# Optimization experiments

Measured on AMD Instinct MI355X. Metric: run time of the kernel, lower is better.

Reference implementation:

```python
import jax, jax.numpy as jnp
import numpy as np

NODES = 14      # input_size: nodes per graph
IN_F = 24       # seq_len: node feature dim
HID1 = 32
HID2 = 64       # hid_feats
HEADS = 2
OUT = 24        # output_size
B = 2048        # number of graphs
SLOPE = 0.2


def _make_edges():
    # fully connected (no self loops) within each 14-node graph
    pairs = np.array([(i, j) for i in range(NODES) for j in range(NODES) if i != j]).T  # [2,182]
    offs = (np.arange(B) * NODES)[:, None]
    src = (pairs[0][None, :] + offs).reshape(-1)
    dst = (pairs[1][None, :] + offs).reshape(-1)
    return np.stack([src, dst]).astype(np.int32)  # [2, 372736]


def setup_inputs() -> dict:
    key = jax.random.key(0)
    ks = jax.random.split(key, 16)
    N = B * NODES
    x = jax.random.normal(ks[0], (N, IN_F), dtype=jnp.float32)
    y = jax.random.normal(ks[1], (N, OUT), dtype=jnp.float32)
    edge_index = jnp.asarray(_make_edges())
    batch = jnp.repeat(jnp.arange(B, dtype=jnp.int32), NODES)
    s = 0.1
    params = dict(
        W1=jax.random.normal(ks[2], (IN_F, HEADS * HID1), dtype=jnp.float32) * s,
        a_src1=jax.random.normal(ks[3], (HEADS, HID1), dtype=jnp.float32) * s,
        a_dst1=jax.random.normal(ks[4], (HEADS, HID1), dtype=jnp.float32) * s,
        b1=jnp.zeros((HID1,), dtype=jnp.float32),
        W2=jax.random.normal(ks[5], (HID1, HEADS * HID2), dtype=jnp.float32) * s,
        a_src2=jax.random.normal(ks[6], (HEADS, HID2), dtype=jnp.float32) * s,
        a_dst2=jax.random.normal(ks[7], (HEADS, HID2), dtype=jnp.float32) * s,
        b2=jnp.zeros((HID2,), dtype=jnp.float32),
        Wf1=jax.random.normal(ks[8], (NODES, HID2, 8), dtype=jnp.float32) * s,
        bf1=jnp.zeros((NODES, 8), dtype=jnp.float32),
        Wf2=jax.random.normal(ks[9], (NODES, 8, OUT), dtype=jnp.float32) * s,
        bf2=jnp.zeros((NODES, OUT), dtype=jnp.float32),
    )
    return {"x": x, "y": y, "edge_index": edge_index, "batch": batch, **params}


def gat_conv(x, src, dst, W, a_src, a_dst, b):
    # PyG GATConv, concat=False (mean over heads), self-loops already in src/dst
    N = x.shape[0]
    H, F = a_src.shape
    xh = (x @ W).reshape(N, H, F)                       # [N,H,F]
    al_s = (xh * a_src).sum(-1)                         # [N,H]
    al_d = (xh * a_dst).sum(-1)                         # [N,H]
    alpha = jax.nn.leaky_relu(al_s[src] + al_d[dst], SLOPE)  # [E,H]
    amax = jax.ops.segment_max(alpha, dst, num_segments=N)
    ex = jnp.exp(alpha - amax[dst])
    den = jax.ops.segment_sum(ex, dst, num_segments=N)
    w = ex / den[dst]                                   # softmax per target node
    out = jax.ops.segment_sum(w[:, :, None] * xh[src], dst, num_segments=N)  # [N,H,F]
    return out.mean(axis=1) + b


def reference(x, y, edge_index, batch, W1, a_src1, a_dst1, b1, W2, a_src2, a_dst2, b2, Wf1, bf1, Wf2, bf2):
    N = x.shape[0]
    loops = jnp.arange(N, dtype=edge_index.dtype)
    src = jnp.concatenate([edge_index[0], loops])
    dst = jnp.concatenate([edge_index[1], loops])
    h = jax.nn.elu(gat_conv(x, src, dst, W1, a_src1, a_dst1, b1))   # [N,32]
    h = gat_conv(h, src, dst, W2, a_src2, a_dst2, b2)               # [N,64]
    # batch regroup: batch ids are contiguous per graph, so the Python
    # gather-loop in the original is exactly a reshape
    nb = N // NODES
    xg = h.reshape(nb, NODES, HID2).transpose(1, 0, 2)   # [14, B, 64]
    yg = y.reshape(nb, NODES, OUT)                       # [B, 14, out]
    # per-node-index MLP ensemble, batched over the 14 indices
    hh = jax.nn.relu(jnp.einsum('kbh,kho->kbo', xg, Wf1) + bf1[:, None, :])
    pred = jax.nn.sigmoid(jnp.einsum('kbo,kop->kbp', hh, Wf2) + bf2[:, None, :])  # [14,B,out]
    return pred, yg
```

## Files before the change

### kernel.cpp

```cpp
#include <hip/hip_runtime.h>

#define NODES 14
#define IN_F 24
#define HID1 32
#define HID2 64
#define OUT_F 24
#define SLOPE 0.2f

#define XS_S 28
#define H1_S 36
#define H2_S 68

#define U_US1 0
#define U_UD1 48
#define U_US2 96
#define U_UD2 160
#define U_TOT 224

#define PHASE_FENCE() __builtin_amdgcn_sched_barrier(0)

__global__ __launch_bounds__(256) void compute_uvecs(
    const float* __restrict__ W1, const float* __restrict__ a_src1,
    const float* __restrict__ a_dst1,
    const float* __restrict__ W2, const float* __restrict__ a_src2,
    const float* __restrict__ a_dst2, float* __restrict__ u)
{
  const int tid = threadIdx.x;
  if (tid < 96) {
    const int sd = (tid >= 48), r = tid - sd * 48;
    const int h = (r >= IN_F), k = r - h * IN_F;
    const float* av = sd ? a_dst1 : a_src1;
    float s = 0.f;
#pragma unroll
    for (int f = 0; f < HID1; ++f)
      s += W1[k * 64 + h * HID1 + f] * av[h * HID1 + f];
    u[(sd ? U_UD1 : U_US1) + h * IN_F + k] = s;
  } else if (tid < 224) {
    const int j = tid - 96;
    const int sd = (j >= 64), r = j - sd * 64;
    const int h = (r >= HID1), k = r - h * HID1;
    const float* av = sd ? a_dst2 : a_src2;
    float s = 0.f;
#pragma unroll
    for (int f = 0; f < HID2; ++f)
      s += W2[k * 128 + h * HID2 + f] * av[h * HID2 + f];
    u[(sd ? U_UD2 : U_US2) + h * HID1 + k] = s;
  }
}

__global__ __launch_bounds__(128) void gnn_fused(
    const float* __restrict__ x, const float* __restrict__ y,
    const float* __restrict__ W1, const float* __restrict__ b1,
    const float* __restrict__ W2, const float* __restrict__ b2,
    const float* __restrict__ Wf1, const float* __restrict__ bf1,
    const float* __restrict__ Wf2, const float* __restrict__ bf2,
    const float* __restrict__ uvec,
    float* __restrict__ out, int ngraphs)
{
  const int g = blockIdx.x;
  const int tid = threadIdx.x;
  const int lane = tid & 63;
  const int wid = tid >> 6;

  __shared__ float u[U_TOT];
  __shared__ __align__(16) float xs[NODES * XS_S];
  __shared__ __align__(16) float h1s[NODES * H1_S];
  __shared__ float h2s[NODES * H2_S];
  __shared__ float watt[NODES * 28];
  __shared__ float als[28], ald[28];
  __shared__ float hhs[112];

  if (tid < (NODES * OUT_F) / 4) {
    const float4* y4 = (const float4*)(y + (size_t)g * (NODES * OUT_F));
    float4* o4 = (float4*)(out + (size_t)NODES * ngraphs * OUT_F
                               + (size_t)g * (NODES * OUT_F));
    o4[tid] = y4[tid];
  }
  for (int i = tid; i < U_TOT; i += 128) u[i] = uvec[i];
  if (tid < (NODES * IN_F) / 4) {
    const float4 v = *(const float4*)(x + (size_t)g * (NODES * IN_F) + tid * 4);
    const int n = (tid * 4) / IN_F, k = (tid * 4) - n * IN_F;
    *(float4*)&xs[n * XS_S + k] = v;
  }
  __syncthreads();
  PHASE_FENCE();

  float xcol[NODES];
  {
    float w[IN_F];
#pragma unroll
    for (int k = 0; k < IN_F; ++k) w[k] = W1[k * 64 + lane];
#pragma unroll 2
    for (int n = 0; n < NODES; ++n) {
      float acc = 0.f;
#pragma unroll
      for (int k4 = 0; k4 < IN_F / 4; ++k4) {
        const float4 xv = *(const float4*)&xs[n * XS_S + k4 * 4];
        acc += xv.x * w[k4 * 4 + 0] + xv.y * w[k4 * 4 + 1]
             + xv.z * w[k4 * 4 + 2] + xv.w * w[k4 * 4 + 3];
      }
      xcol[n] = acc;
    }
  }
  PHASE_FENCE();

  if (tid < 56) {
    const int n = tid >> 2, h = (tid >> 1) & 1, sd = tid & 1;
    const float* uu = u + (sd ? U_UD1 : U_US1) + h * IN_F;
    float s = 0.f;
#pragma unroll
    for (int k = 0; k < IN_F; ++k) s += xs[n * XS_S + k] * uu[k];
    (sd ? ald : als)[n * 2 + h] = s;
  }
  __syncthreads();
  PHASE_FENCE();

  if (tid < NODES * 2) {
    const int h = tid & 1;
    const float ad = ald[tid];
    float a[NODES]; float m = -1e30f;
#pragma unroll
    for (int i = 0; i < NODES; ++i) {
      float v = als[i * 2 + h] + ad;
      v = v > 0.f ? v : SLOPE * v;
      a[i] = v; m = fmaxf(m, v);
    }
    float den = 0.f;
#pragma unroll
    for (int i = 0; i < NODES; ++i) { a[i] = __expf(a[i] - m); den += a[i]; }
    const float r = 1.f / den;
#pragma unroll
    for (int i = 0; i < NODES; ++i) watt[i * 28 + tid] = a[i] * r;
  }
  __syncthreads();
  PHASE_FENCE();

  {
    const int h = lane >> 5, f5 = lane & 31;
    const float bb = b1[f5];
#pragma unroll 2
    for (int tt = 0; tt < NODES / 2; ++tt) {
      const int n = wid * (NODES / 2) + tt;
      float o = 0.f;
#pragma unroll
      for (int i = 0; i < NODES; ++i)
        o += watt[i * 28 + n * 2 + h] * xcol[i];
      const float oo = __shfl_xor(o, 32);
      if (h == 0) {
        const float v = 0.5f * (o + oo) + bb;
        h1s[n * H1_S + f5] = v > 0.f ? v : expm1f(v);
      }
    }
  }
  __syncthreads();
  PHASE_FENCE();

  float x2c[NODES];
  {
    float w2[HID1];
#pragma unroll
    for (int k = 0; k < HID1; ++k) w2[k] = W2[k * 128 + tid];
#pragma unroll 2
    for (int n = 0; n < NODES; ++n) {
      float acc = 0.f;
#pragma unroll
      for (int k4 = 0; k4 < HID1 / 4; ++k4) {
        const float4 hv = *(const float4*)&h1s[n * H1_S + k4 * 4];
        acc += hv.x * w2[k4 * 4 + 0] + hv.y * w2[k4 * 4 + 1]
             + hv.z * w2[k4 * 4 + 2] + hv.w * w2[k4 * 4 + 3];
      }
      x2c[n] = acc;
    }
  }
  PHASE_FENCE();

  if (tid < 56) {
    const int n = tid >> 2, h = (tid >> 1) & 1, sd = tid & 1;
    const float* uu = u + (sd ? U_UD2 : U_US2) + h * HID1;
    float s = 0.f;
#pragma unroll
    for (int k = 0; k < HID1; ++k) s += h1s[n * H1_S + k] * uu[k];
    (sd ? ald : als)[n * 2 + h] = s;
  }
  __syncthreads();
  PHASE_FENCE();

  if (tid < NODES * 2) {
    const int h = tid & 1;
    const float ad = ald[tid];
    float a[NODES]; float m = -1e30f;
#pragma unroll
    for (int i = 0; i < NODES; ++i) {
      float v = als[i * 2 + h] + ad;
      v = v > 0.f ? v : SLOPE * v;
      a[i] = v; m = fmaxf(m, v);
    }
    float den = 0.f;
#pragma unroll
    for (int i = 0; i < NODES; ++i) { a[i] = __expf(a[i] - m); den += a[i]; }
    const float r = 1.f / den;
#pragma unroll
    for (int i = 0; i < NODES; ++i) watt[i * 28 + tid] = a[i] * r;
  }
  __syncthreads();
  PHASE_FENCE();

  {
    float agg[NODES];
#pragma unroll
    for (int n = 0; n < NODES; ++n) {
      float o = 0.f;
#pragma unroll
      for (int i = 0; i < NODES; ++i)
        o += watt[i * 28 + n * 2 + wid] * x2c[i];
      agg[n] = o;
    }
    if (wid == 1) {
#pragma unroll
      for (int n = 0; n < NODES; ++n) h2s[n * H2_S + lane] = agg[n];
    }
    __syncthreads();
    if (wid == 0) {
      const float bb = b2[lane];
#pragma unroll
      for (int n = 0; n < NODES; ++n)
        h2s[n * H2_S + lane] = 0.5f * (agg[n] + h2s[n * H2_S + lane]) + bb;
    }
  }
  __syncthreads();
  PHASE_FENCE();

  if (tid < NODES * 8) {
    const int k = tid >> 3, e = tid & 7;
    float acc = bf1[k * 8 + e];
#pragma unroll 8
    for (int f = 0; f < HID2; ++f)
      acc += h2s[k * H2_S + f] * Wf1[(k * HID2 + f) * 8 + e];
    hhs[tid] = fmaxf(acc, 0.f);
  }
  __syncthreads();
  PHASE_FENCE();

  for (int idx = tid; idx < NODES * OUT_F; idx += 128) {
    const int k = idx / OUT_F, o = idx - k * OUT_F;
    float acc = bf2[k * OUT_F + o];
#pragma unroll
    for (int e = 0; e < 8; ++e)
      acc += hhs[k * 8 + e] * Wf2[(k * 8 + e) * OUT_F + o];
    out[(size_t)k * ngraphs * OUT_F + (size_t)g * OUT_F + o] =
        1.f / (1.f + __expf(-acc));
  }
}

extern "C" void kernel_launch(void* const* d_in, const int* in_sizes, int n_in,
                              void* d_out, int out_size, void* d_ws, size_t ws_size,
                              hipStream_t stream) {
  const float* x      = (const float*)d_in[0];
  const float* y      = (const float*)d_in[1];
  const float* W1     = (const float*)d_in[4];
  const float* a_src1 = (const float*)d_in[5];
  const float* a_dst1 = (const float*)d_in[6];
  const float* b1     = (const float*)d_in[7];
  const float* W2     = (const float*)d_in[8];
  const float* a_src2 = (const float*)d_in[9];
  const float* a_dst2 = (const float*)d_in[10];
  const float* b2     = (const float*)d_in[11];
  const float* Wf1    = (const float*)d_in[12];
  const float* bf1    = (const float*)d_in[13];
  const float* Wf2    = (const float*)d_in[14];
  const float* bf2    = (const float*)d_in[15];
  float* out = (float*)d_out;
  float* u   = (float*)d_ws;

  const int nnodes  = in_sizes[0] / IN_F;
  const int ngraphs = nnodes / NODES;

  hipLaunchKernelGGL(compute_uvecs, dim3(1), dim3(256), 0, stream,
                     W1, a_src1, a_dst1, W2, a_src2, a_dst2, u);
  hipLaunchKernelGGL(gnn_fused, dim3(ngraphs), dim3(128), 0, stream,
                     x, y, W1, b1, W2, b2, Wf1, bf1, Wf2, bf2, u, out, ngraphs);
}
```

Measured before the change: 31.54 us.

## Use 256-thread blocks with node-split work and a shared-memory arena

Block size goes from 128 to 256 threads, and every stage is re-split across four waves. In each GAT layer, the feature transform now goes to shared memory instead of per-thread registers, and the aggregation is split by destination node across waves. The attention-logit dots run on the last wave in the same phase as the transform, which removes a barrier. The aim is more parallelism and latency hiding per graph, at the cost of more LDS traffic and larger blocks that may lower occupancy.

```diff
diff --git a/kernel.cpp b/kernel.cpp
--- a/kernel.cpp
+++ b/kernel.cpp
@@ -7,15 +7,28 @@
 #define OUT_F 24
 #define SLOPE 0.2f
 
-#define XS_S 28
-#define H1_S 36
-#define H2_S 68
-
 #define U_US1 0
 #define U_UD1 48
 #define U_US2 96
 #define U_UD2 160
 #define U_TOT 224
+
+#define A_XS   0
+#define A_XH2  0
+#define XS_S   28
+#define XH2_S  129
+#define A_XH1  1808
+#define A_H2S  1808
+#define XH1_S  65
+#define H2_S   68
+#define A_H1S  2760
+#define H1_S   36
+#define A_WATT 3264
+#define A_ALS  3656
+#define A_ALD  3684
+#define A_HHS  3712
+#define A_U    3824
+#define ARENA  4048
 
 #define PHASE_FENCE() __builtin_amdgcn_sched_barrier(0)
 
@@ -48,7 +61,7 @@
   }
 }
 
-__global__ __launch_bounds__(128) void gnn_fused(
+__global__ __launch_bounds__(256) void gnn_fused(
     const float* __restrict__ x, const float* __restrict__ y,
     const float* __restrict__ W1, const float* __restrict__ b1,
     const float* __restrict__ W2, const float* __restrict__ b2,
@@ -62,13 +75,7 @@
   const int lane = tid & 63;
   const int wid = tid >> 6;
 
-  __shared__ float u[U_TOT];
-  __shared__ __align__(16) float xs[NODES * XS_S];
-  __shared__ __align__(16) float h1s[NODES * H1_S];
-  __shared__ float h2s[NODES * H2_S];
-  __shared__ float watt[NODES * 28];
-  __shared__ float als[28], ald[28];
-  __shared__ float hhs[112];
+  __shared__ __align__(16) float sm[ARENA];
 
   if (tid < (NODES * OUT_F) / 4) {
     const float4* y4 = (const float4*)(y + (size_t)g * (NODES * OUT_F));
@@ -76,52 +83,54 @@
                                + (size_t)g * (NODES * OUT_F));
     o4[tid] = y4[tid];
   }
-  for (int i = tid; i < U_TOT; i += 128) u[i] = uvec[i];
-  if (tid < (NODES * IN_F) / 4) {
-    const float4 v = *(const float4*)(x + (size_t)g * (NODES * IN_F) + tid * 4);
-    const int n = (tid * 4) / IN_F, k = (tid * 4) - n * IN_F;
-    *(float4*)&xs[n * XS_S + k] = v;
-  }
-  __syncthreads();
-  PHASE_FENCE();
-
-  float xcol[NODES];
-  {
+  if (tid >= 128 && tid < 128 + (NODES * IN_F) / 4) {
+    const int idx = tid - 128;
+    const float4 v = *(const float4*)(x + (size_t)g * (NODES * IN_F) + idx * 4);
+    const int n = (idx * 4) / IN_F, k = (idx * 4) - n * IN_F;
+    *(float4*)&sm[A_XS + n * XS_S + k] = v;
+  }
+  if (tid < U_TOT) sm[A_U + tid] = uvec[tid];
+  __syncthreads();
+  PHASE_FENCE();
+
+  {
+    const int col = lane;
     float w[IN_F];
 #pragma unroll
-    for (int k = 0; k < IN_F; ++k) w[k] = W1[k * 64 + lane];
-#pragma unroll 2
-    for (int n = 0; n < NODES; ++n) {
-      float acc = 0.f;
-#pragma unroll
-      for (int k4 = 0; k4 < IN_F / 4; ++k4) {
-        const float4 xv = *(const float4*)&xs[n * XS_S + k4 * 4];
-        acc += xv.x * w[k4 * 4 + 0] + xv.y * w[k4 * 4 + 1]
-             + xv.z * w[k4 * 4 + 2] + xv.w * w[k4 * 4 + 3];
-      }
-      xcol[n] = acc;
-    }
-  }
-  PHASE_FENCE();
-
-  if (tid < 56) {
-    const int n = tid >> 2, h = (tid >> 1) & 1, sd = tid & 1;
-    const float* uu = u + (sd ? U_UD1 : U_US1) + h * IN_F;
-    float s = 0.f;
-#pragma unroll
-    for (int k = 0; k < IN_F; ++k) s += xs[n * XS_S + k] * uu[k];
-    (sd ? ald : als)[n * 2 + h] = s;
+    for (int k = 0; k < IN_F; ++k) w[k] = W1[k * 64 + col];
+#pragma unroll
+    for (int t = 0; t < 4; ++t) {
+      const int n = wid * 4 + t;
+      if (n < NODES) {
+        float acc = 0.f;
+#pragma unroll
+        for (int k4 = 0; k4 < IN_F / 4; ++k4) {
+          const float4 xv = *(const float4*)&sm[A_XS + n * XS_S + k4 * 4];
+          acc += xv.x * w[k4 * 4 + 0] + xv.y * w[k4 * 4 + 1]
+               + xv.z * w[k4 * 4 + 2] + xv.w * w[k4 * 4 + 3];
+        }
+        sm[A_XH1 + n * XH1_S + col] = acc;
+      }
+    }
+    if (wid == 3 && lane < 56) {
+      const int n = lane >> 2, h = (lane >> 1) & 1, sd = lane & 1;
+      const float* uu = &sm[A_U + (sd ? U_UD1 : U_US1) + h * IN_F];
+      float s = 0.f;
+#pragma unroll
+      for (int k = 0; k < IN_F; ++k) s += sm[A_XS + n * XS_S + k] * uu[k];
+      sm[(sd ? A_ALD : A_ALS) + n * 2 + h] = s;
+    }
   }
   __syncthreads();
   PHASE_FENCE();
 
   if (tid < NODES * 2) {
     const int h = tid & 1;
-    const float ad = ald[tid];
+    const float ad = sm[A_ALD + tid];
     float a[NODES]; float m = -1e30f;
 #pragma unroll
     for (int i = 0; i < NODES; ++i) {
-      float v = als[i * 2 + h] + ad;
+      float v = sm[A_ALS + i * 2 + h] + ad;
       v = v > 0.f ? v : SLOPE * v;
       a[i] = v; m = fmaxf(m, v);
     }
@@ -130,68 +139,77 @@
     for (int i = 0; i < NODES; ++i) { a[i] = __expf(a[i] - m); den += a[i]; }
     const float r = 1.f / den;
 #pragma unroll
-    for (int i = 0; i < NODES; ++i) watt[i * 28 + tid] = a[i] * r;
-  }
-  __syncthreads();
-  PHASE_FENCE();
-
-  {
-    const int h = lane >> 5, f5 = lane & 31;
+    for (int i = 0; i < NODES; ++i) sm[A_WATT + i * 28 + tid] = a[i] * r;
+  }
+  __syncthreads();
+  PHASE_FENCE();
+
+  {
+    const int f5 = lane & 31, h = lane >> 5;
     const float bb = b1[f5];
-#pragma unroll 2
-    for (int tt = 0; tt < NODES / 2; ++tt) {
-      const int n = wid * (NODES / 2) + tt;
-      float o = 0.f;
-#pragma unroll
-      for (int i = 0; i < NODES; ++i)
-        o += watt[i * 28 + n * 2 + h] * xcol[i];
-      const float oo = __shfl_xor(o, 32);
-      if (h == 0) {
-        const float v = 0.5f * (o + oo) + bb;
-        h1s[n * H1_S + f5] = v > 0.f ? v : expm1f(v);
-      }
-    }
-  }
-  __syncthreads();
-  PHASE_FENCE();
-
-  float x2c[NODES];
-  {
-    float w2[HID1];
-#pragma unroll
-    for (int k = 0; k < HID1; ++k) w2[k] = W2[k * 128 + tid];
-#pragma unroll 2
-    for (int n = 0; n < NODES; ++n) {
-      float acc = 0.f;
-#pragma unroll
-      for (int k4 = 0; k4 < HID1 / 4; ++k4) {
-        const float4 hv = *(const float4*)&h1s[n * H1_S + k4 * 4];
-        acc += hv.x * w2[k4 * 4 + 0] + hv.y * w2[k4 * 4 + 1]
+#pragma unroll
+    for (int t = 0; t < 4; ++t) {
+      const int n = wid * 4 + t;
+      if (n < NODES) {
+        float o = 0.f;
+#pragma unroll
+        for (int i = 0; i < NODES; ++i)
+          o += sm[A_WATT + i * 28 + n * 2 + h] * sm[A_XH1 + i * XH1_S + lane];
+        const float oo = __shfl_xor(o, 32);
+        if (h == 0) {
+          const float v = 0.5f * (o + oo) + bb;
+          sm[A_H1S + n * H1_S + f5] = v > 0.f ? v : expm1f(v);
+        }
+      }
+    }
+  }
+  __syncthreads();
+  PHASE_FENCE();
+
+  {
+    const int col2 = tid & 127;
+    const int nb = (tid >> 7) * 7;
+    float acc[7] = {0.f, 0.f, 0.f, 0.f, 0.f, 0.f, 0.f};
+#pragma unroll
+    for (int c = 0; c < 2; ++c) {
+      float w2[16];
+#pragma unroll
+      for (int k = 0; k < 16; ++k) w2[k] = W2[(c * 16 + k) * 128 + col2];
+#pragma unroll
+      for (int t = 0; t < 7; ++t) {
+        const int n = nb + t;
+        float a = 0.f;
+#pragma unroll
+        for (int k4 = 0; k4 < 4; ++k4) {
+          const float4 hv = *(const float4*)&sm[A_H1S + n * H1_S + c * 16 + k4 * 4];
+          a += hv.x * w2[k4 * 4 + 0] + hv.y * w2[k4 * 4 + 1]
              + hv.z * w2[k4 * 4 + 2] + hv.w * w2[k4 * 4 + 3];
-      }
-      x2c[n] = acc;
-    }
-  }
-  PHASE_FENCE();
-
-  if (tid < 56) {
-    const int n = tid >> 2, h = (tid >> 1) & 1, sd = tid & 1;
-    const float* uu = u + (sd ? U_UD2 : U_US2) + h * HID1;
-    float s = 0.f;
-#pragma unroll
-    for (int k = 0; k < HID1; ++k) s += h1s[n * H1_S + k] * uu[k];
-    (sd ? ald : als)[n * 2 + h] = s;
+        }
+        acc[t] += a;
+      }
+    }
+#pragma unroll
+    for (int t = 0; t < 7; ++t)
+      sm[A_XH2 + (nb + t) * XH2_S + col2] = acc[t];
+    if (wid == 3 && lane < 56) {
+      const int n = lane >> 2, h = (lane >> 1) & 1, sd = lane & 1;
+      const float* uu = &sm[A_U + (sd ? U_UD2 : U_US2) + h * HID1];
+      float s = 0.f;
+#pragma unroll
+      for (int k = 0; k < HID1; ++k) s += sm[A_H1S + n * H1_S + k] * uu[k];
+      sm[(sd ? A_ALD : A_ALS) + n * 2 + h] = s;
+    }
   }
   __syncthreads();
   PHASE_FENCE();
 
   if (tid < NODES * 2) {
     const int h = tid & 1;
-    const float ad = ald[tid];
+    const float ad = sm[A_ALD + tid];
     float a[NODES]; float m = -1e30f;
 #pragma unroll
     for (int i = 0; i < NODES; ++i) {
-      float v = als[i * 2 + h] + ad;
+      float v = sm[A_ALS + i * 2 + h] + ad;
       v = v > 0.f ? v : SLOPE * v;
       a[i] = v; m = fmaxf(m, v);
     }
@@ -200,53 +218,50 @@
     for (int i = 0; i < NODES; ++i) { a[i] = __expf(a[i] - m); den += a[i]; }
     const float r = 1.f / den;
 #pragma unroll
-    for (int i = 0; i < NODES; ++i) watt[i * 28 + tid] = a[i] * r;
-  }
-  __syncthreads();
-  PHASE_FENCE();
-
-  {
-    float agg[NODES];
-#pragma unroll
-    for (int n = 0; n < NODES; ++n) {
-      float o = 0.f;
-#pragma unroll
-      for (int i = 0; i < NODES; ++i)
-        o += watt[i * 28 + n * 2 + wid] * x2c[i];
-      agg[n] = o;
-    }
-    if (wid == 1) {
-#pragma unroll
-      for (int n = 0; n < NODES; ++n) h2s[n * H2_S + lane] = agg[n];
-    }
-    __syncthreads();
-    if (wid == 0) {
-      const float bb = b2[lane];
-#pragma unroll
-      for (int n = 0; n < NODES; ++n)
-        h2s[n * H2_S + lane] = 0.5f * (agg[n] + h2s[n * H2_S + lane]) + bb;
-    }
-  }
-  __syncthreads();
-  PHASE_FENCE();
-
-  if (tid < NODES * 8) {
-    const int k = tid >> 3, e = tid & 7;
-    float acc = bf1[k * 8 + e];
-#pragma unroll 8
-    for (int f = 0; f < HID2; ++f)
-      acc += h2s[k * H2_S + f] * Wf1[(k * HID2 + f) * 8 + e];
-    hhs[tid] = fmaxf(acc, 0.f);
-  }
-  __syncthreads();
-  PHASE_FENCE();
-
-  for (int idx = tid; idx < NODES * OUT_F; idx += 128) {
+    for (int i = 0; i < NODES; ++i) sm[A_WATT + i * 28 + tid] = a[i] * r;
+  }
+  __syncthreads();
+  PHASE_FENCE();
+
+  {
+    const float bb = b2[lane];
+#pragma unroll
+    for (int t = 0; t < 4; ++t) {
+      const int n = wid * 4 + t;
+      if (n < NODES) {
+        float o0 = 0.f, o1 = 0.f;
+#pragma unroll
+        for (int i = 0; i < NODES; ++i) {
+          o0 += sm[A_WATT + i * 28 + n * 2 + 0] * sm[A_XH2 + i * XH2_S + lane];
+          o1 += sm[A_WATT + i * 28 + n * 2 + 1] * sm[A_XH2 + i * XH2_S + 64 + lane];
+        }
+        sm[A_H2S + n * H2_S + lane] = 0.5f * (o0 + o1) + bb;
+      }
+    }
+  }
+  __syncthreads();
+  PHASE_FENCE();
+
+  if (tid < 224) {
+    const int item = tid >> 1, k = item >> 3, e = item & 7, half = tid & 1;
+    float p = 0.f;
+#pragma unroll
+    for (int f = 0; f < 32; ++f)
+      p += sm[A_H2S + k * H2_S + half * 32 + f]
+         * Wf1[(k * HID2 + half * 32 + f) * 8 + e];
+    const float pp = __shfl_xor(p, 1);
+    if (half == 0)
+      sm[A_HHS + item] = fmaxf(p + pp + bf1[k * 8 + e], 0.f);
+  }
+  __syncthreads();
+  PHASE_FENCE();
+
+  for (int idx = tid; idx < NODES * OUT_F; idx += 256) {
     const int k = idx / OUT_F, o = idx - k * OUT_F;
     float acc = bf2[k * OUT_F + o];
 #pragma unroll
     for (int e = 0; e < 8; ++e)
-      acc += hhs[k * 8 + e] * Wf2[(k * 8 + e) * OUT_F + o];
+      acc += sm[A_HHS + k * 8 + e] * Wf2[(k * 8 + e) * OUT_F + o];
     out[(size_t)k * ngraphs * OUT_F + (size_t)g * OUT_F + o] =
         1.f / (1.f + __expf(-acc));
   }
@@ -277,6 +292,6 @@
 
   hipLaunchKernelGGL(compute_uvecs, dim3(1), dim3(256), 0, stream,
                      W1, a_src1, a_dst1, W2, a_src2, a_dst2, u);
-  hipLaunchKernelGGL(gnn_fused, dim3(ngraphs), dim3(128), 0, stream,
+  hipLaunchKernelGGL(gnn_fused, dim3(ngraphs), dim3(256), 0, stream,
                      x, y, W1, b1, W2, b2, Wf1, bf1, Wf2, bf2, u, out, ngraphs);
 }
```

After: 35.21 us. +11.6%, slower.

## Prefetch weights early and split layer-2 aggregation by head per wave

Applied to the files above, without the earlier changes.

W1, W2 and half of Wf1 are now loaded into registers ahead of the barriers, so their global-load latency overlaps earlier phases. Each thread computes both heads' layer-2 projections for its feature lane, which lets the aggregation split nodes across the two waves and removes a barrier plus a shared-memory round trip for head averaging. The cost is higher register pressure from the extra live arrays, which could lower occupancy or cause spills.

```diff
diff --git a/kernel.cpp b/kernel.cpp
--- a/kernel.cpp
+++ b/kernel.cpp
@@ -70,6 +70,10 @@
   __shared__ float als[28], ald[28];
   __shared__ float hhs[112];
 
+  float w1r[IN_F];
+#pragma unroll
+  for (int k = 0; k < IN_F; ++k) w1r[k] = W1[k * 64 + lane];
+
   if (tid < (NODES * OUT_F) / 4) {
     const float4* y4 = (const float4*)(y + (size_t)g * (NODES * OUT_F));
     float4* o4 = (float4*)(out + (size_t)NODES * ngraphs * OUT_F
@@ -87,17 +91,14 @@
 
   float xcol[NODES];
   {
-    float w[IN_F];
-#pragma unroll
-    for (int k = 0; k < IN_F; ++k) w[k] = W1[k * 64 + lane];
 #pragma unroll 2
     for (int n = 0; n < NODES; ++n) {
       float acc = 0.f;
 #pragma unroll
       for (int k4 = 0; k4 < IN_F / 4; ++k4) {
         const float4 xv = *(const float4*)&xs[n * XS_S + k4 * 4];
-        acc += xv.x * w[k4 * 4 + 0] + xv.y * w[k4 * 4 + 1]
-             + xv.z * w[k4 * 4 + 2] + xv.w * w[k4 * 4 + 3];
+        acc += xv.x * w1r[k4 * 4 + 0] + xv.y * w1r[k4 * 4 + 1]
+             + xv.z * w1r[k4 * 4 + 2] + xv.w * w1r[k4 * 4 + 3];
       }
       xcol[n] = acc;
     }
@@ -115,6 +116,9 @@
   __syncthreads();
   PHASE_FENCE();
 
+  float w2a[HID1];
+#pragma unroll
+  for (int k = 0; k < HID1; ++k) w2a[k] = W2[k * 128 + lane];
   if (tid < NODES * 2) {
     const int h = tid & 1;
     const float ad = ald[tid];
@@ -155,21 +159,32 @@
   __syncthreads();
   PHASE_FENCE();
 
-  float x2c[NODES];
-  {
-    float w2[HID1];
-#pragma unroll
-    for (int k = 0; k < HID1; ++k) w2[k] = W2[k * 128 + tid];
+  float x2c0[NODES], x2c1[NODES];
+  {
 #pragma unroll 2
     for (int n = 0; n < NODES; ++n) {
       float acc = 0.f;
 #pragma unroll
       for (int k4 = 0; k4 < HID1 / 4; ++k4) {
         const float4 hv = *(const float4*)&h1s[n * H1_S + k4 * 4];
-        acc += hv.x * w2[k4 * 4 + 0] + hv.y * w2[k4 * 4 + 1]
-             + hv.z * w2[k4 * 4 + 2] + hv.w * w2[k4 * 4 + 3];
-      }
-      x2c[n] = acc;
+        acc += hv.x * w2a[k4 * 4 + 0] + hv.y * w2a[k4 * 4 + 1]
+             + hv.z * w2a[k4 * 4 + 2] + hv.w * w2a[k4 * 4 + 3];
+      }
+      x2c0[n] = acc;
+    }
+    float w2b[HID1];
+#pragma unroll
+    for (int k = 0; k < HID1; ++k) w2b[k] = W2[k * 128 + 64 + lane];
+#pragma unroll 2
+    for (int n = 0; n < NODES; ++n) {
+      float acc = 0.f;
+#pragma unroll
+      for (int k4 = 0; k4 < HID1 / 4; ++k4) {
+        const float4 hv = *(const float4*)&h1s[n * H1_S + k4 * 4];
+        acc += hv.x * w2b[k4 * 4 + 0] + hv.y * w2b[k4 * 4 + 1]
+             + hv.z * w2b[k4 * 4 + 2] + hv.w * w2b[k4 * 4 + 3];
+      }
+      x2c1[n] = acc;
     }
   }
   PHASE_FENCE();
@@ -185,6 +200,12 @@
   __syncthreads();
   PHASE_FENCE();
 
+  float wf[32];
+  if (tid < NODES * 8) {
+    const int k = tid >> 3, e = tid & 7;
+#pragma unroll
+    for (int f = 0; f < 32; ++f) wf[f] = Wf1[(k * HID2 + f) * 8 + e];
+  }
   if (tid < NODES * 2) {
     const int h = tid & 1;
     const float ad = ald[tid];
@@ -206,25 +227,18 @@
   PHASE_FENCE();
 
   {
-    float agg[NODES];
-#pragma unroll
-    for (int n = 0; n < NODES; ++n) {
-      float o = 0.f;
-#pragma unroll
-      for (int i = 0; i < NODES; ++i)
-        o += watt[i * 28 + n * 2 + wid] * x2c[i];
-      agg[n] = o;
-    }
-    if (wid == 1) {
-#pragma unroll
-      for (int n = 0; n < NODES; ++n) h2s[n * H2_S + lane] = agg[n];
-    }
-    __syncthreads();
-    if (wid == 0) {
-      const float bb = b2[lane];
-#pragma unroll
-      for (int n = 0; n < NODES; ++n)
-        h2s[n * H2_S + lane] = 0.5f * (agg[n] + h2s[n * H2_S + lane]) + bb;
+    const float bb = b2[lane];
+#pragma unroll 2
+    for (int tt = 0; tt < NODES / 2; ++tt) {
+      const int n = wid * (NODES / 2) + tt;
+      float o0 = 0.f, o1 = 0.f;
+#pragma unroll
+      for (int i = 0; i < NODES; ++i) {
+        const float2 wv = *(const float2*)&watt[i * 28 + n * 2];
+        o0 += wv.x * x2c0[i];
+        o1 += wv.y * x2c1[i];
+      }
+      h2s[n * H2_S + lane] = 0.5f * (o0 + o1) + bb;
     }
   }
   __syncthreads();
@@ -233,8 +247,11 @@
   if (tid < NODES * 8) {
     const int k = tid >> 3, e = tid & 7;
     float acc = bf1[k * 8 + e];
+#pragma unroll
+    for (int f = 0; f < 32; ++f)
+      acc += h2s[k * H2_S + f] * wf[f];
 #pragma unroll 8
-    for (int f = 0; f < HID2; ++f)
+    for (int f = 32; f < HID2; ++f)
       acc += h2s[k * H2_S + f] * Wf1[(k * HID2 + f) * 8 + e];
     hhs[tid] = fmaxf(acc, 0.f);
   }
```

Result: slower. 46.30 us (+46.8%).

## Use 256-thread blocks and overlap attention softmax with projection matmuls

Applied to the files above, without the earlier changes.

Doubles the block to 256 threads and reassigns the work: each thread computes a few nodes for a few feature columns of both heads, and partial aggregations are reduced across lanes with shuffles. Wave 0 now computes the attention logits and softmax while the other waves run the x@W projection, which removes two barriers per layer. The Wf1 stage splits its reduction over two threads. This adds more cross-lane shuffle reductions, higher register pressure and fewer resident blocks per CU.

```diff
diff --git a/kernel.cpp b/kernel.cpp
--- a/kernel.cpp
+++ b/kernel.cpp
@@ -48,7 +48,7 @@
   }
 }
 
-__global__ __launch_bounds__(128) void gnn_fused(
+__global__ __launch_bounds__(256) void gnn_fused(
     const float* __restrict__ x, const float* __restrict__ y,
     const float* __restrict__ W1, const float* __restrict__ b1,
     const float* __restrict__ W2, const float* __restrict__ b2,
@@ -60,14 +60,14 @@
   const int g = blockIdx.x;
   const int tid = threadIdx.x;
   const int lane = tid & 63;
-  const int wid = tid >> 6;
+  const int wv = tid >> 6;
 
   __shared__ float u[U_TOT];
   __shared__ __align__(16) float xs[NODES * XS_S];
+  __shared__ float als[28], ald[28];
+  __shared__ float watt[NODES * 28];
   __shared__ __align__(16) float h1s[NODES * H1_S];
   __shared__ float h2s[NODES * H2_S];
-  __shared__ float watt[NODES * 28];
-  __shared__ float als[28], ald[28];
   __shared__ float hhs[112];
 
   if (tid < (NODES * OUT_F) / 4) {
@@ -75,173 +75,203 @@
     float4* o4 = (float4*)(out + (size_t)NODES * ngraphs * OUT_F
                                + (size_t)g * (NODES * OUT_F));
     o4[tid] = y4[tid];
-  }
-  for (int i = tid; i < U_TOT; i += 128) u[i] = uvec[i];
-  if (tid < (NODES * IN_F) / 4) {
-    const float4 v = *(const float4*)(x + (size_t)g * (NODES * IN_F) + tid * 4);
-    const int n = (tid * 4) / IN_F, k = (tid * 4) - n * IN_F;
+  } else if (tid < 168) {
+    const int idx = tid - 84;
+    const float4 v = *(const float4*)(x + (size_t)g * (NODES * IN_F) + idx * 4);
+    const int n = (idx * 4) / IN_F, k = (idx * 4) - n * IN_F;
     *(float4*)&xs[n * XS_S + k] = v;
   }
-  __syncthreads();
-  PHASE_FENCE();
-
-  float xcol[NODES];
+  if (tid < U_TOT) u[tid] = uvec[tid];
+  __syncthreads();
+  PHASE_FENCE();
+
+  if (wv == 0) {
+    if (lane < 56) {
+      const int n = lane >> 2, h = (lane >> 1) & 1, sd = lane & 1;
+      const float* uu = u + (sd ? U_UD1 : U_US1) + h * IN_F;
+      float s = 0.f;
+#pragma unroll
+      for (int k = 0; k < IN_F; ++k) s += xs[n * XS_S + k] * uu[k];
+      (sd ? ald : als)[n * 2 + h] = s;
+    }
+    if (lane < NODES * 2) {
+      const int h = lane & 1;
+      const float ad = ald[lane];
+      float a[NODES]; float m = -1e30f;
+#pragma unroll
+      for (int i = 0; i < NODES; ++i) {
+        float v = als[i * 2 + h] + ad;
+        v = v > 0.f ? v : SLOPE * v;
+        a[i] = v; m = fmaxf(m, v);
+      }
+      float den = 0.f;
+#pragma unroll
+      for (int i = 0; i < NODES; ++i) { a[i] = __expf(a[i] - m); den += a[i]; }
+      const float r = 1.f / den;
+#pragma unroll
+      for (int i = 0; i < NODES; ++i) watt[i * 28 + lane] = a[i] * r;
+    }
+  }
+  const int f8 = (wv << 3) | (lane & 7);
+  const int g8 = lane >> 3;
+  float xc[2][2] = {{0.f, 0.f}, {0.f, 0.f}};
+  if (g8 < 7) {
+#pragma unroll
+    for (int c = 0; c < 2; ++c) {
+      const int col = c * HID1 + f8;
+      float wr[IN_F];
+#pragma unroll
+      for (int k = 0; k < IN_F; ++k) wr[k] = W1[k * 64 + col];
+#pragma unroll
+      for (int t = 0; t < 2; ++t) {
+        const int n = g8 * 2 + t;
+        float acc = 0.f;
+#pragma unroll
+        for (int k4 = 0; k4 < IN_F / 4; ++k4) {
+          const float4 xv = *(const float4*)&xs[n * XS_S + k4 * 4];
+          acc += xv.x * wr[k4 * 4 + 0] + xv.y * wr[k4 * 4 + 1]
+               + xv.z * wr[k4 * 4 + 2] + xv.w * wr[k4 * 4 + 3];
+        }
+        xc[c][t] = acc;
+      }
+      PHASE_FENCE();
+    }
+  }
+  __syncthreads();
+  PHASE_FENCE();
+
   {
-    float w[IN_F];
-#pragma unroll
-    for (int k = 0; k < IN_F; ++k) w[k] = W1[k * 64 + lane];
-#pragma unroll 2
+    float q[NODES];
+#pragma unroll
     for (int n = 0; n < NODES; ++n) {
-      float acc = 0.f;
-#pragma unroll
-      for (int k4 = 0; k4 < IN_F / 4; ++k4) {
-        const float4 xv = *(const float4*)&xs[n * XS_S + k4 * 4];
-        acc += xv.x * w[k4 * 4 + 0] + xv.y * w[k4 * 4 + 1]
-             + xv.z * w[k4 * 4 + 2] + xv.w * w[k4 * 4 + 3];
-      }
-      xcol[n] = acc;
-    }
-  }
-  PHASE_FENCE();
-
-  if (tid < 56) {
-    const int n = tid >> 2, h = (tid >> 1) & 1, sd = tid & 1;
-    const float* uu = u + (sd ? U_UD1 : U_US1) + h * IN_F;
+      float s = 0.f;
+      if (g8 < 7) {
+#pragma unroll
+        for (int t = 0; t < 2; ++t) {
+          const int i = g8 * 2 + t;
+          const float2 wv2 = *(const float2*)&watt[i * 28 + n * 2];
+          s += wv2.x * xc[0][t] + wv2.y * xc[1][t];
+        }
+      }
+      q[n] = s;
+    }
+#pragma unroll
+    for (int n = 0; n < NODES; ++n) q[n] += __shfl_xor(q[n], 8);
+#pragma unroll
+    for (int n = 0; n < NODES; ++n) q[n] += __shfl_xor(q[n], 16);
+#pragma unroll
+    for (int n = 0; n < NODES; ++n) q[n] += __shfl_xor(q[n], 32);
+    if (g8 < 7) {
+      const float bb = b1[f8];
+#pragma unroll
+      for (int t = 0; t < 2; ++t) {
+        const int n = g8 * 2 + t;
+        const float v = 0.5f * q[n] + bb;
+        h1s[n * H1_S + f8] = v > 0.f ? v : expm1f(v);
+      }
+    }
+  }
+  __syncthreads();
+  PHASE_FENCE();
+
+  if (wv == 0) {
+    if (lane < 56) {
+      const int n = lane >> 2, h = (lane >> 1) & 1, sd = lane & 1;
+      const float* uu = u + (sd ? U_UD2 : U_US2) + h * HID1;
+      float s = 0.f;
+#pragma unroll
+      for (int k = 0; k < HID1; ++k) s += h1s[n * H1_S + k] * uu[k];
+      (sd ? ald : als)[n * 2 + h] = s;
+    }
+    if (lane < NODES * 2) {
+      const int h = lane & 1;
+      const float ad = ald[lane];
+      float a[NODES]; float m = -1e30f;
+#pragma unroll
+      for (int i = 0; i < NODES; ++i) {
+        float v = als[i * 2 + h] + ad;
+        v = v > 0.f ? v : SLOPE * v;
+        a[i] = v; m = fmaxf(m, v);
+      }
+      float den = 0.f;
+#pragma unroll
+      for (int i = 0; i < NODES; ++i) { a[i] = __expf(a[i] - m); den += a[i]; }
+      const float r = 1.f / den;
+#pragma unroll
+      for (int i = 0; i < NODES; ++i) watt[i * 28 + lane] = a[i] * r;
+    }
+  }
+  const int f16 = (wv << 4) | (lane & 15);
+  const int g4 = lane >> 4;
+  const int nb = g4 * 4;
+  float x2[2][4] = {{0.f,0.f,0.f,0.f},{0.f,0.f,0.f,0.f}};
+#pragma unroll
+  for (int c = 0; c < 2; ++c) {
+    const int col = c * HID2 + f16;
+    float w2[HID1];
+#pragma unroll
+    for (int k = 0; k < HID1; ++k) w2[k] = W2[k * 128 + col];
+#pragma unroll
+    for (int t = 0; t < 4; ++t) {
+      const int n = nb + t;
+      if (n < NODES) {
+        float acc = 0.f;
+#pragma unroll
+        for (int k4 = 0; k4 < HID1 / 4; ++k4) {
+          const float4 hv = *(const float4*)&h1s[n * H1_S + k4 * 4];
+          acc += hv.x * w2[k4 * 4 + 0] + hv.y * w2[k4 * 4 + 1]
+               + hv.z * w2[k4 * 4 + 2] + hv.w * w2[k4 * 4 + 3];
+        }
+        x2[c][t] = acc;
+      }
+    }
+    PHASE_FENCE();
+  }
+  __syncthreads();
+  PHASE_FENCE();
+
+  {
+    float q2[NODES];
+#pragma unroll
+    for (int n = 0; n < NODES; ++n) {
+      float s = 0.f;
+#pragma unroll
+      for (int t = 0; t < 4; ++t) {
+        const int i = nb + t;
+        if (i < NODES) {
+          const float2 wv2 = *(const float2*)&watt[i * 28 + n * 2];
+          s += wv2.x * x2[0][t] + wv2.y * x2[1][t];
+        }
+      }
+      q2[n] = s;
+    }
+#pragma unroll
+    for (int n = 0; n < NODES; ++n) q2[n] += __shfl_xor(q2[n], 16);
+#pragma unroll
+    for (int n = 0; n < NODES; ++n) q2[n] += __shfl_xor(q2[n], 32);
+    const float bb = b2[f16];
+#pragma unroll
+    for (int t = 0; t < 4; ++t) {
+      const int n = nb + t;
+      if (n < NODES) h2s[n * H2_S + f16] = 0.5f * q2[n] + bb;
+    }
+  }
+  __syncthreads();
+  PHASE_FENCE();
+
+  if (tid < 224) {
+    const int item = tid >> 1, k = item >> 3, e = item & 7, hf = tid & 1;
     float s = 0.f;
 #pragma unroll
-    for (int k = 0; k < IN_F; ++k) s += xs[n * XS_S + k] * uu[k];
-    (sd ? ald : als)[n * 2 + h] = s;
-  }
-  __syncthreads();
-  PHASE_FENCE();
-
-  if (tid < NODES * 2) {
-    const int h = tid & 1;
-    const float ad = ald[tid];
-    float a[NODES]; float m = -1e30f;
-#pragma unroll
-    for (int i = 0; i < NODES; ++i) {
-      float v = als[i * 2 + h] + ad;
-      v = v > 0.f ? v : SLOPE * v;
-      a[i] = v; m = fmaxf(m, v);
-    }
-    float den = 0.f;
-#pragma unroll
-    for (int i = 0; i < NODES; ++i) { a[i] = __expf(a[i] - m); den += a[i]; }
-    const float r = 1.f / den;
-#pragma unroll
-    for (int i = 0; i < NODES; ++i) watt[i * 28 + tid] = a[i] * r;
-  }
-  __syncthreads();
-  PHASE_FENCE();
-
-  {
-    const int h = lane >> 5, f5 = lane & 31;
-    const float bb = b1[f5];
-#pragma unroll 2
-    for (int tt = 0; tt < NODES / 2; ++tt) {
-      const int n = wid * (NODES / 2) + tt;
-      float o = 0.f;
-#pragma unroll
-      for (int i = 0; i < NODES; ++i)
-        o += watt[i * 28 + n * 2 + h] * xcol[i];
-      const float oo = __shfl_xor(o, 32);
-      if (h == 0) {
-        const float v = 0.5f * (o + oo) + bb;
-        h1s[n * H1_S + f5] = v > 0.f ? v : expm1f(v);
-      }
-    }
-  }
-  __syncthreads();
-  PHASE_FENCE();
-
-  float x2c[NODES];
-  {
-    float w2[HID1];
-#pragma unroll
-    for (int k = 0; k < HID1; ++k) w2[k] = W2[k * 128 + tid];
-#pragma unroll 2
-    for (int n = 0; n < NODES; ++n) {
-      float acc = 0.f;
-#pragma unroll
-      for (int k4 = 0; k4 < HID1 / 4; ++k4) {
-        const float4 hv = *(const float4*)&h1s[n * H1_S + k4 * 4];
-        acc += hv.x * w2[k4 * 4 + 0] + hv.y * w2[k4 * 4 + 1]
-             + hv.z * w2[k4 * 4 + 2] + hv.w * w2[k4 * 4 + 3];
-      }
-      x2c[n] = acc;
-    }
-  }
-  PHASE_FENCE();
-
-  if (tid < 56) {
-    const int n = tid >> 2, h = (tid >> 1) & 1, sd = tid & 1;
-    const float* uu = u + (sd ? U_UD2 : U_US2) + h * HID1;
-    float s = 0.f;
-#pragma unroll
-    for (int k = 0; k < HID1; ++k) s += h1s[n * H1_S + k] * uu[k];
-    (sd ? ald : als)[n * 2 + h] = s;
-  }
-  __syncthreads();
-  PHASE_FENCE();
-
-  if (tid < NODES * 2) {
-    const int h = tid & 1;
-    const float ad = ald[tid];
-    float a[NODES]; float m = -1e30f;
-#pragma unroll
-    for (int i = 0; i < NODES; ++i) {
-      float v = als[i * 2 + h] + ad;
-      v = v > 0.f ? v : SLOPE * v;
-      a[i] = v; m = fmaxf(m, v);
-    }
-    float den = 0.f;
-#pragma unroll
-    for (int i = 0; i < NODES; ++i) { a[i] = __expf(a[i] - m); den += a[i]; }
-    const float r = 1.f / den;
-#pragma unroll
-    for (int i = 0; i < NODES; ++i) watt[i * 28 + tid] = a[i] * r;
-  }
-  __syncthreads();
-  PHASE_FENCE();
-
-  {
-    float agg[NODES];
-#pragma unroll
-    for (int n = 0; n < NODES; ++n) {
-      float o = 0.f;
-#pragma unroll
-      for (int i = 0; i < NODES; ++i)
-        o += watt[i * 28 + n * 2 + wid] * x2c[i];
-      agg[n] = o;
-    }
-    if (wid == 1) {
-#pragma unroll
-      for (int n = 0; n < NODES; ++n) h2s[n * H2_S + lane] = agg[n];
-    }
-    __syncthreads();
-    if (wid == 0) {
-      const float bb = b2[lane];
-#pragma unroll
-      for (int n = 0; n < NODES; ++n)
-        h2s[n * H2_S + lane] = 0.5f * (agg[n] + h2s[n * H2_S + lane]) + bb;
-    }
-  }
-  __syncthreads();
-  PHASE_FENCE();
-
-  if (tid < NODES * 8) {
-    const int k = tid >> 3, e = tid & 7;
-    float acc = bf1[k * 8 + e];
-#pragma unroll 8
-    for (int f = 0; f < HID2; ++f)
-      acc += h2s[k * H2_S + f] * Wf1[(k * HID2 + f) * 8 + e];
-    hhs[tid] = fmaxf(acc, 0.f);
-  }
-  __syncthreads();
-  PHASE_FENCE();
-
-  for (int idx = tid; idx < NODES * OUT_F; idx += 128) {
+    for (int f = 0; f < 32; ++f)
+      s += h2s[k * H2_S + hf * 32 + f] * Wf1[(k * HID2 + hf * 32 + f) * 8 + e];
+    const float ss = __shfl_xor(s, 1);
+    if (hf == 0) hhs[item] = fmaxf(s + ss + bf1[k * 8 + e], 0.f);
+  }
+  __syncthreads();
+  PHASE_FENCE();
+
+  for (int idx = tid; idx < NODES * OUT_F; idx += 256) {
     const int k = idx / OUT_F, o = idx - k * OUT_F;
     float acc = bf2[k * OUT_F + o];
 #pragma unroll
@@ -277,6 +307,6 @@
 
   hipLaunchKernelGGL(compute_uvecs, dim3(1), dim3(256), 0, stream,
                      W1, a_src1, a_dst1, W2, a_src2, a_dst2, u);
-  hipLaunchKernelGGL(gnn_fused, dim3(ngraphs), dim3(128), 0, stream,
+  hipLaunchKernelGGL(gnn_fused, dim3(ngraphs), dim3(256), 0, stream,
                      x, y, W1, b1, W2, b2, Wf1, bf1, Wf2, bf2, u, out, ngraphs);
 }
```

Result: slower. 93.21 us (+195.6%).
